# Kernel optimization log

Hardware: AMD Instinct MI355X
Metric: run time of the kernel (lower is better)

## Reference

```python
import jax, jax.numpy as jnp
import numpy as np

B, D = 8192, 128


def setup_inputs() -> dict:
    key = jax.random.key(0)
    ks = jax.random.split(key, 7)
    s = 1.0 / np.sqrt(D)  # torch Linear default init scale
    x = jax.random.normal(ks[0], (B, D), jnp.float32)
    W1 = jax.random.uniform(ks[1], (D, D), jnp.float32, -s, s)
    b1 = jax.random.uniform(ks[2], (D,), jnp.float32, -s, s)
    Wmu = jax.random.uniform(ks[3], (D, D), jnp.float32, -s, s)
    bmu = jax.random.uniform(ks[4], (D,), jnp.float32, -s, s)
    Wls = jax.random.uniform(ks[5], (D, D), jnp.float32, -s, s)
    bls = jax.random.uniform(ks[6], (D,), jnp.float32, -s, s)
    return {"x": x, "W1": W1, "b1": b1, "Wmu": Wmu, "bmu": bmu, "Wls": Wls, "bls": bls}


def reference(x, W1, b1, Wmu, bmu, Wls, bls):
    d = x.shape[1]
    mask = jnp.tril(jnp.ones((d, d), x.dtype), -1)  # strict lower triangular, as in MaskedLinear
    W1m = W1 * mask
    Wmum = Wmu * mask
    Wlsm = Wls * mask

    def step(carry, i):
        z, ldj = carry
        h = jax.nn.relu(z @ W1m.T + b1)          # [B, D] hidden (MaskedLinear + ReLU)
        # only column i of mu/logs is consumed each step -> use weight row i
        mu_i = h @ Wmum[i] + bmu[i]              # [B]
        logs_i = h @ Wlsm[i] + bls[i]            # [B]
        z = z.at[:, i].set(mu_i + x[:, i] * jnp.exp(logs_i))
        return (z, ldj + logs_i), None

    z0 = jnp.zeros_like(x)
    ldj0 = jnp.zeros(x.shape[0], x.dtype)
    (z, ldj), _ = jax.lax.scan(step, (z0, ldj0), jnp.arange(d))
    return z, ldj
```

## Files before the change

kernel.cpp:

```cpp
#include <hip/hip_runtime.h>
#include <stdint.h>

#define D 128
#define LOG2E 1.4426950408889634f
#define LN2 0.6931471805599453f

typedef float f2 __attribute__((ext_vector_type(2)));
typedef float f4 __attribute__((ext_vector_type(4)));

__device__ __forceinline__ uint16_t f2bf(float f) {
  uint32_t u = __float_as_uint(f);
  u += 0x7fffu + ((u >> 16) & 1u);
  return (uint16_t)(u >> 16);
}
__device__ __forceinline__ uint32_t pkbf(float a, float b) {
  return (uint32_t)f2bf(a) | ((uint32_t)f2bf(b) << 16);
}
__device__ __forceinline__ f2 unpkbf(uint32_t u) {
  f2 r;
  r.x = __uint_as_float(u << 16);
  r.y = __uint_as_float(u & 0xffff0000u);
  return r;
}
__device__ __forceinline__ float rdlane(float v, int l) {
  return __int_as_float(__builtin_amdgcn_readlane(__float_as_int(v), l));
}
__device__ __forceinline__ float exp2x(float v) {
#if __has_builtin(__builtin_amdgcn_exp2f)
  return __builtin_amdgcn_exp2f(v);
#else
  return exp2f(v);
#endif
}

#define WS_NEED (size_t)(3 * 2048 * 16)

__global__ __launch_bounds__(256)
void iaf_prep(const float* __restrict__ W1, const float* __restrict__ Wmu,
              const float* __restrict__ Wls, uint4* __restrict__ ws) {
  const int t = blockIdx.x * 256 + threadIdx.x;
  if (t >= 32 * 64) return;
  const int jb = t >> 6, l = t & 63;
  const int k0 = 2 * l, k1 = 2 * l + 1;
  uint32_t mm[4], ll[4], ww[4];
#pragma unroll
  for (int c = 0; c < 4; ++c) {
    const int j = jb * 4 + c;
    const float m0 = (j < k0) ? Wmu[k0 * D + j] : 0.f;
    const float m1 = (j < k1) ? Wmu[k1 * D + j] : 0.f;
    const float s0 = (j < k0) ? Wls[k0 * D + j] * LOG2E : 0.f;
    const float s1 = (j < k1) ? Wls[k1 * D + j] * LOG2E : 0.f;
    const float w0 = (j < k0) ? W1[k0 * D + j] : 0.f;
    const float w1_ = (j < k1) ? W1[k1 * D + j] : 0.f;
    mm[c] = pkbf(m0, m1);
    ll[c] = pkbf(s0, s1);
    ww[c] = pkbf(w0, w1_);
  }
  uint4 m4, l4, w4;
  m4.x = mm[0]; m4.y = mm[1]; m4.z = mm[2]; m4.w = mm[3];
  l4.x = ll[0]; l4.y = ll[1]; l4.z = ll[2]; l4.w = ll[3];
  w4.x = ww[0]; w4.y = ww[1]; w4.z = ww[2]; w4.w = ww[3];
  ws[t] = m4;
  ws[2048 + t] = l4;
  ws[4096 + t] = w4;
}

#define SEL(U, c) ((c) == 0 ? (U).x : (c) == 1 ? (U).y : (c) == 2 ? (U).z : (U).w)
#define E(V, c) (((c) & 1) ? (V).y : (V).x)

#define STEP(c)                                                         \
  {                                                                     \
    const int Ln = jb * 2 + ((c) >> 1);                                 \
    const f2 wm = unpkbf(SEL(mC, c));                                   \
    const f2 wl = unpkbf(SEL(lC, c));                                   \
    const f2 wv = unpkbf(SEL(wC, c));                                   \
    const float hA = fmaxf(E(paA, c), 0.f);                             \
    const float hB = fmaxf(E(paB, c), 0.f);                             \
    const float zA = fmaf(E(xA, c), exp2x(E(plsA, c)), E(pmuA, c));     \
    const float zB = fmaf(E(xB, c), exp2x(E(plsB, c)), E(pmuB, c));     \
    const float szA = rdlane(zA, Ln);                                   \
    const float shA = rdlane(hA, Ln);                                   \
    const float szB = rdlane(zB, Ln);                                   \
    const float shB = rdlane(hB, Ln);                                   \
    paA = __builtin_elementwise_fma((f2)szA, wv, paA);                  \
    pmuA = __builtin_elementwise_fma((f2)shA, wm, pmuA);                \
    plsA = __builtin_elementwise_fma((f2)shA, wl, plsA);                \
    paB = __builtin_elementwise_fma((f2)szB, wv, paB);                  \
    pmuB = __builtin_elementwise_fma((f2)shB, wm, pmuB);                \
    plsB = __builtin_elementwise_fma((f2)shB, wl, plsB);                \
  }

__global__ __launch_bounds__(512, 4)
void iaf_main(const float* __restrict__ x, const float* __restrict__ b1,
              const float* __restrict__ bmu, const float* __restrict__ bls,
              const uint4* __restrict__ ws, float* __restrict__ out, int B) {
  __shared__ uint4 wsh[2 * 2048];

  const int tid = threadIdx.x;
#pragma unroll
  for (int k = 0; k < 8; ++k) wsh[tid + k * 512] = ws[tid + k * 512];

  const int lane = tid & 63;
  const int wave = tid >> 6;
  const int rA = blockIdx.x * 16 + wave * 2;
  const int rB = rA + 1;
  const int l2 = lane * 2;

  const f2 xA = *(const f2*)(x + (size_t)rA * D + l2);
  const f2 xB = *(const f2*)(x + (size_t)rB * D + l2);
  f2 paA = *(const f2*)(b1 + l2);
  f2 paB = paA;
  f2 pmuA = *(const f2*)(bmu + l2);
  f2 pmuB = pmuA;
  f2 plsA = *(const f2*)(bls + l2);
  plsA.x *= LOG2E;
  plsA.y *= LOG2E;
  f2 plsB = plsA;

  const uint4* wmuP = wsh + lane;
  const uint4* wlsP = wsh + 2048 + lane;
  const uint4* w1P = ws + 4096 + lane;

  __syncthreads();

  uint4 mC = wmuP[0], lC = wlsP[0], wC = w1P[0];

#pragma unroll 1
  for (int jb = 0; jb < 32; ++jb) {
    const int adv = (jb + 1 < 32) ? 64 : 0;
    wmuP += adv;
    wlsP += adv;
    w1P += adv;
    const uint4 mN = wmuP[0];
    const uint4 lN = wlsP[0];
    const uint4 wN = w1P[0];
    STEP(0)
    STEP(1)
    STEP(2)
    STEP(3)
    mC = mN;
    lC = lN;
    wC = wN;
  }

  f2 zfA, zfB;
  zfA.x = fmaf(xA.x, exp2x(plsA.x), pmuA.x);
  zfA.y = fmaf(xA.y, exp2x(plsA.y), pmuA.y);
  zfB.x = fmaf(xB.x, exp2x(plsB.x), pmuB.x);
  zfB.y = fmaf(xB.y, exp2x(plsB.y), pmuB.y);
  *(f2*)(out + (size_t)rA * D + l2) = zfA;
  *(f2*)(out + (size_t)rB * D + l2) = zfB;

  float ldjA = plsA.x + plsA.y;
  float ldjB = plsB.x + plsB.y;
#pragma unroll
  for (int m2 = 1; m2 < 64; m2 <<= 1) {
    ldjA += __shfl_xor(ldjA, m2);
    ldjB += __shfl_xor(ldjB, m2);
  }
  if (lane == 0) {
    out[(size_t)B * D + rA] = ldjA * LN2;
    out[(size_t)B * D + rB] = ldjB * LN2;
  }
}

#define FNTHR 256
#define FRPB 16
#define W1S 136
template <int CTRL>
__device__ __forceinline__ float dppmov(float v) {
  return __int_as_float(
      __builtin_amdgcn_update_dpp(0, __float_as_int(v), CTRL, 0xf, 0xf, true));
}
#define DPP_ADD(v, ctrl) (v) += dppmov<(ctrl)>((v))
__device__ __forceinline__ f2 unpk(uint32_t u) {
  f2 r;
  r.x = __uint_as_float(u << 16);
  r.y = __uint_as_float(u & 0xffff0000u);
  return r;
}
#define RED16F(v)      \
  do {                 \
    DPP_ADD(v, 0xB1);  \
    DPP_ADD(v, 0x4E);  \
    DPP_ADD(v, 0x124); \
    DPP_ADD(v, 0x128); \
  } while (0)
#define FSTEP(I, XE, ZRE, MKE, WM0, WM1, WL0, WL1)                  \
  {                                                                 \
    const float bmu_i = bmu[(I)];                                   \
    const float bls_i = bls[(I)];                                   \
    const f2 h0 = __builtin_elementwise_max(A0, (f2)0.f);           \
    const f2 h1 = __builtin_elementwise_max(A1, (f2)0.f);           \
    const f2 h2_ = __builtin_elementwise_max(A2, (f2)0.f);          \
    const f2 h3 = __builtin_elementwise_max(A3, (f2)0.f);           \
    const f2 q0 = h0 * mk0, q1 = h1 * mk1;                          \
    const f2 q2 = h2_ * mk2, q3 = h3 * mk3;                         \
    f2 am = q0 * WM0.xy;                                            \
    f2 al = q0 * WL0.xy;                                            \
    am = __builtin_elementwise_fma(q1, WM0.zw, am);                 \
    al = __builtin_elementwise_fma(q1, WL0.zw, al);                 \
    am = __builtin_elementwise_fma(q2, WM1.xy, am);                 \
    al = __builtin_elementwise_fma(q2, WL1.xy, al);                 \
    am = __builtin_elementwise_fma(q3, WM1.zw, am);                 \
    al = __builtin_elementwise_fma(q3, WL1.zw, al);                 \
    float mu_p = am.x + am.y;                                       \
    float ls_p = al.x + al.y;                                       \
    {                                                               \
      const int pfr = ((I) + 2 < D) ? (I) + 2 : D - 1;              \
      WM0 = *(const f4*)(wmup + pfr * D);                           \
      WM1 = *(const f4*)(wmup + pfr * D + 4);                       \
      WL0 = *(const f4*)(wlsp + pfr * D);                           \
      WL1 = *(const f4*)(wlsp + pfr * D + 4);                       \
    }                                                               \
    RED16F(mu_p);                                                   \
    RED16F(ls_p);                                                   \
    const float mu_t = mu_p + bmu_i;                                \
    const float ls_t = ls_p + bls_i;                                \
    const float zi = fmaf((XE), __expf(ls_t), mu_t);                \
    ldj += ls_t;                                                    \
    const uint4 wv = *(const uint4*)(w1p + (I)*W1S);                \
    if (own) {                                                      \
      ZRE = zi;                                                     \
      MKE = 1.f;                                                    \
    }                                                               \
    f2 zz;                                                          \
    zz.x = zi;                                                      \
    zz.y = zi;                                                      \
    A0 = __builtin_elementwise_fma(zz, unpk(wv.x), A0);             \
    A1 = __builtin_elementwise_fma(zz, unpk(wv.y), A1);             \
    A2 = __builtin_elementwise_fma(zz, unpk(wv.z), A2);             \
    A3 = __builtin_elementwise_fma(zz, unpk(wv.w), A3);             \
  }

__global__ __launch_bounds__(FNTHR, 2)
void iaf_fb(const float* __restrict__ x, const float* __restrict__ W1,
            const float* __restrict__ b1, const float* __restrict__ Wmu,
            const float* __restrict__ bmu, const float* __restrict__ Wls,
            const float* __restrict__ bls, float* __restrict__ out, int B) {
  __shared__ uint16_t w1c[D * W1S];
  const int tid = threadIdx.x;
  for (int idx = tid; idx < D * D; idx += FNTHR) {
    const int p = idx >> 7, q = idx & (D - 1);
    w1c[q * W1S + p] = f2bf((p > q) ? W1[idx] : 0.f);
  }
  __syncthreads();
  const int lane = tid & 63;
  const int m = lane & 15;
  const int row = blockIdx.x * FRPB + (tid >> 4);
  const float* __restrict__ xp = x + (size_t)row * D;
  const float* __restrict__ wmup = Wmu + m * 8;
  const float* __restrict__ wlsp = Wls + m * 8;
  const uint16_t* __restrict__ w1p = w1c + m * 8;
  f2 A0, A1, A2, A3;
  {
    const f4 t0 = *(const f4*)(b1 + m * 8);
    const f4 t1 = *(const f4*)(b1 + m * 8 + 4);
    A0 = t0.xy; A1 = t0.zw; A2 = t1.xy; A3 = t1.zw;
  }
  f2 mk0 = (f2)0.f, mk1 = (f2)0.f, mk2 = (f2)0.f, mk3 = (f2)0.f;
  float zr0 = 0, zr1 = 0, zr2 = 0, zr3 = 0, zr4 = 0, zr5 = 0, zr6 = 0, zr7 = 0;
  float ldj = 0.f;
  f4 wmA0 = *(const f4*)(wmup);
  f4 wmA1 = *(const f4*)(wmup + 4);
  f4 wlA0 = *(const f4*)(wlsp);
  f4 wlA1 = *(const f4*)(wlsp + 4);
  f4 wmB0 = *(const f4*)(wmup + D);
  f4 wmB1 = *(const f4*)(wmup + D + 4);
  f4 wlB0 = *(const f4*)(wlsp + D);
  f4 wlB1 = *(const f4*)(wlsp + D + 4);
  f4 x4a = *(const f4*)(xp);
  f4 x4b;
  for (int ib = 0; ib < 16; ++ib) {
    const int i0 = ib * 8;
    const bool own = (m == ib);
    x4b = *(const f4*)(xp + i0 + 4);
    FSTEP(i0 + 0, x4a.x, zr0, mk0.x, wmA0, wmA1, wlA0, wlA1);
    FSTEP(i0 + 1, x4a.y, zr1, mk0.y, wmB0, wmB1, wlB0, wlB1);
    FSTEP(i0 + 2, x4a.z, zr2, mk1.x, wmA0, wmA1, wlA0, wlA1);
    FSTEP(i0 + 3, x4a.w, zr3, mk1.y, wmB0, wmB1, wlB0, wlB1);
    {
      const int nx = (i0 + 8 < D) ? i0 + 8 : D - 4;
      x4a = *(const f4*)(xp + nx);
    }
    FSTEP(i0 + 4, x4b.x, zr4, mk2.x, wmA0, wmA1, wlA0, wlA1);
    FSTEP(i0 + 5, x4b.y, zr5, mk2.y, wmB0, wmB1, wlB0, wlB1);
    FSTEP(i0 + 6, x4b.z, zr6, mk3.x, wmA0, wmA1, wlA0, wlA1);
    FSTEP(i0 + 7, x4b.w, zr7, mk3.y, wmB0, wmB1, wlB0, wlB1);
  }
  f4 o0, o1;
  o0.x = zr0; o0.y = zr1; o0.z = zr2; o0.w = zr3;
  o1.x = zr4; o1.y = zr5; o1.z = zr6; o1.w = zr7;
  float* zo = out + (size_t)row * D + m * 8;
  *(f4*)(zo) = o0;
  *(f4*)(zo + 4) = o1;
  if (m == 0) out[(size_t)B * D + row] = ldj;
}

extern "C" void kernel_launch(void* const* d_in, const int* in_sizes, int n_in,
                              void* d_out, int out_size, void* d_ws, size_t ws_size,
                              hipStream_t stream) {
  const float* x   = (const float*)d_in[0];
  const float* W1  = (const float*)d_in[1];
  const float* b1  = (const float*)d_in[2];
  const float* Wmu = (const float*)d_in[3];
  const float* bmu = (const float*)d_in[4];
  const float* Wls = (const float*)d_in[5];
  const float* bls = (const float*)d_in[6];
  float* out = (float*)d_out;

  const int B = in_sizes[0] / D;

  if (ws_size >= WS_NEED) {
    iaf_prep<<<8, 256, 0, stream>>>(W1, Wmu, Wls, (uint4*)d_ws);
    const int grid = (B + 15) / 16;
    iaf_main<<<grid, 512, 0, stream>>>(x, b1, bmu, bls, (const uint4*)d_ws, out, B);
  } else {
    const int grid = (B + FRPB - 1) / FRPB;
    iaf_fb<<<grid, FNTHR, 0, stream>>>(x, W1, b1, Wmu, bmu, Wls, bls, out, B);
  }
}
```

Before: 39.22 us.

## Process four rows per wave and double-buffer weight loads per iteration

```diff
diff --git a/kernel.cpp b/kernel.cpp
--- a/kernel.cpp
+++ b/kernel.cpp
@@ -68,29 +68,43 @@
 #define SEL(U, c) ((c) == 0 ? (U).x : (c) == 1 ? (U).y : (c) == 2 ? (U).z : (U).w)
 #define E(V, c) (((c) & 1) ? (V).y : (V).x)
 
-#define STEP(c)                                                         \
-  {                                                                     \
-    const int Ln = jb * 2 + ((c) >> 1);                                 \
-    const f2 wm = unpkbf(SEL(mC, c));                                   \
-    const f2 wl = unpkbf(SEL(lC, c));                                   \
-    const f2 wv = unpkbf(SEL(wC, c));                                   \
-    const float hA = fmaxf(E(paA, c), 0.f);                             \
-    const float hB = fmaxf(E(paB, c), 0.f);                             \
-    const float zA = fmaf(E(xA, c), exp2x(E(plsA, c)), E(pmuA, c));     \
-    const float zB = fmaf(E(xB, c), exp2x(E(plsB, c)), E(pmuB, c));     \
-    const float szA = rdlane(zA, Ln);                                   \
-    const float shA = rdlane(hA, Ln);                                   \
-    const float szB = rdlane(zB, Ln);                                   \
-    const float shB = rdlane(hB, Ln);                                   \
-    paA = __builtin_elementwise_fma((f2)szA, wv, paA);                  \
-    pmuA = __builtin_elementwise_fma((f2)shA, wm, pmuA);                \
-    plsA = __builtin_elementwise_fma((f2)shA, wl, plsA);                \
-    paB = __builtin_elementwise_fma((f2)szB, wv, paB);                  \
-    pmuB = __builtin_elementwise_fma((f2)shB, wm, pmuB);                \
-    plsB = __builtin_elementwise_fma((f2)shB, wl, plsB);                \
-  }
-
-__global__ __launch_bounds__(512, 4)
+#define STEP(c, M4, L4, W4, JB)                                       \
+  {                                                                   \
+    const int Ln = (JB) * 2 + ((c) >> 1);                             \
+    const f2 wm = unpkbf(SEL(M4, c));                                 \
+    const f2 wl = unpkbf(SEL(L4, c));                                 \
+    const f2 wv = unpkbf(SEL(W4, c));                                 \
+    const float hA = fmaxf(E(paA, c), 0.f);                           \
+    const float hB = fmaxf(E(paB, c), 0.f);                           \
+    const float hC = fmaxf(E(paC, c), 0.f);                           \
+    const float hD = fmaxf(E(paD, c), 0.f);                           \
+    const float zA = fmaf(E(xA, c), exp2x(E(plsA, c)), E(pmuA, c));   \
+    const float zB = fmaf(E(xB, c), exp2x(E(plsB, c)), E(pmuB, c));   \
+    const float zC = fmaf(E(xC, c), exp2x(E(plsC, c)), E(pmuC, c));   \
+    const float zD = fmaf(E(xD, c), exp2x(E(plsD, c)), E(pmuD, c));   \
+    const float szA = rdlane(zA, Ln);                                 \
+    const float shA = rdlane(hA, Ln);                                 \
+    const float szB = rdlane(zB, Ln);                                 \
+    const float shB = rdlane(hB, Ln);                                 \
+    const float szC = rdlane(zC, Ln);                                 \
+    const float shC = rdlane(hC, Ln);                                 \
+    const float szD = rdlane(zD, Ln);                                 \
+    const float shD = rdlane(hD, Ln);                                 \
+    paA = __builtin_elementwise_fma((f2)szA, wv, paA);                \
+    pmuA = __builtin_elementwise_fma((f2)shA, wm, pmuA);              \
+    plsA = __builtin_elementwise_fma((f2)shA, wl, plsA);              \
+    paB = __builtin_elementwise_fma((f2)szB, wv, paB);                \
+    pmuB = __builtin_elementwise_fma((f2)shB, wm, pmuB);              \
+    plsB = __builtin_elementwise_fma((f2)shB, wl, plsB);              \
+    paC = __builtin_elementwise_fma((f2)szC, wv, paC);                \
+    pmuC = __builtin_elementwise_fma((f2)shC, wm, pmuC);              \
+    plsC = __builtin_elementwise_fma((f2)shC, wl, plsC);              \
+    paD = __builtin_elementwise_fma((f2)szD, wv, paD);                \
+    pmuD = __builtin_elementwise_fma((f2)shD, wm, pmuD);              \
+    plsD = __builtin_elementwise_fma((f2)shD, wl, plsD);              \
+  }
+
+__global__ __launch_bounds__(256, 2)
 void iaf_main(const float* __restrict__ x, const float* __restrict__ b1,
               const float* __restrict__ bmu, const float* __restrict__ bls,
               const uint4* __restrict__ ws, float* __restrict__ out, int B) {
@@ -98,24 +112,25 @@
 
   const int tid = threadIdx.x;
 #pragma unroll
-  for (int k = 0; k < 8; ++k) wsh[tid + k * 512] = ws[tid + k * 512];
+  for (int k = 0; k < 16; ++k) wsh[tid + k * 256] = ws[tid + k * 256];
 
   const int lane = tid & 63;
   const int wave = tid >> 6;
-  const int rA = blockIdx.x * 16 + wave * 2;
-  const int rB = rA + 1;
+  const int rA = blockIdx.x * 16 + wave * 4;
   const int l2 = lane * 2;
 
   const f2 xA = *(const f2*)(x + (size_t)rA * D + l2);
-  const f2 xB = *(const f2*)(x + (size_t)rB * D + l2);
+  const f2 xB = *(const f2*)(x + (size_t)(rA + 1) * D + l2);
+  const f2 xC = *(const f2*)(x + (size_t)(rA + 2) * D + l2);
+  const f2 xD = *(const f2*)(x + (size_t)(rA + 3) * D + l2);
   f2 paA = *(const f2*)(b1 + l2);
-  f2 paB = paA;
+  f2 paB = paA, paC = paA, paD = paA;
   f2 pmuA = *(const f2*)(bmu + l2);
-  f2 pmuB = pmuA;
+  f2 pmuB = pmuA, pmuC = pmuA, pmuD = pmuA;
   f2 plsA = *(const f2*)(bls + l2);
   plsA.x *= LOG2E;
   plsA.y *= LOG2E;
-  f2 plsB = plsA;
+  f2 plsB = plsA, plsC = plsA, plsD = plsA;
 
   const uint4* wmuP = wsh + lane;
   const uint4* wlsP = wsh + 2048 + lane;
@@ -123,44 +138,60 @@
 
   __syncthreads();
 
-  uint4 mC = wmuP[0], lC = wlsP[0], wC = w1P[0];
+  uint4 m0 = wmuP[0], l0 = wlsP[0], w0 = w1P[0];
 
 #pragma unroll 1
-  for (int jb = 0; jb < 32; ++jb) {
-    const int adv = (jb + 1 < 32) ? 64 : 0;
+  for (int jb = 0; jb < 32; jb += 2) {
+    const uint4 m1 = wmuP[64];
+    const uint4 l1 = wlsP[64];
+    const uint4 w1v = w1P[64];
+    STEP(0, m0, l0, w0, jb)
+    STEP(1, m0, l0, w0, jb)
+    STEP(2, m0, l0, w0, jb)
+    STEP(3, m0, l0, w0, jb)
+    const int adv = (jb + 2 < 32) ? 128 : 0;
     wmuP += adv;
     wlsP += adv;
     w1P += adv;
-    const uint4 mN = wmuP[0];
-    const uint4 lN = wlsP[0];
-    const uint4 wN = w1P[0];
-    STEP(0)
-    STEP(1)
-    STEP(2)
-    STEP(3)
-    mC = mN;
-    lC = lN;
-    wC = wN;
-  }
-
-  f2 zfA, zfB;
-  zfA.x = fmaf(xA.x, exp2x(plsA.x), pmuA.x);
-  zfA.y = fmaf(xA.y, exp2x(plsA.y), pmuA.y);
-  zfB.x = fmaf(xB.x, exp2x(plsB.x), pmuB.x);
-  zfB.y = fmaf(xB.y, exp2x(plsB.y), pmuB.y);
-  *(f2*)(out + (size_t)rA * D + l2) = zfA;
-  *(f2*)(out + (size_t)rB * D + l2) = zfB;
+    m0 = wmuP[0];
+    l0 = wlsP[0];
+    w0 = w1P[0];
+    STEP(0, m1, l1, w1v, jb + 1)
+    STEP(1, m1, l1, w1v, jb + 1)
+    STEP(2, m1, l1, w1v, jb + 1)
+    STEP(3, m1, l1, w1v, jb + 1)
+  }
+
+  f2 zf;
+  zf.x = fmaf(xA.x, exp2x(plsA.x), pmuA.x);
+  zf.y = fmaf(xA.y, exp2x(plsA.y), pmuA.y);
+  *(f2*)(out + (size_t)rA * D + l2) = zf;
+  zf.x = fmaf(xB.x, exp2x(plsB.x), pmuB.x);
+  zf.y = fmaf(xB.y, exp2x(plsB.y), pmuB.y);
+  *(f2*)(out + (size_t)(rA + 1) * D + l2) = zf;
+  zf.x = fmaf(xC.x, exp2x(plsC.x), pmuC.x);
+  zf.y = fmaf(xC.y, exp2x(plsC.y), pmuC.y);
+  *(f2*)(out + (size_t)(rA + 2) * D + l2) = zf;
+  zf.x = fmaf(xD.x, exp2x(plsD.x), pmuD.x);
+  zf.y = fmaf(xD.y, exp2x(plsD.y), pmuD.y);
+  *(f2*)(out + (size_t)(rA + 3) * D + l2) = zf;
 
   float ldjA = plsA.x + plsA.y;
   float ldjB = plsB.x + plsB.y;
+  float ldjC = plsC.x + plsC.y;
+  float ldjD = plsD.x + plsD.y;
 #pragma unroll
   for (int m2 = 1; m2 < 64; m2 <<= 1) {
     ldjA += __shfl_xor(ldjA, m2);
     ldjB += __shfl_xor(ldjB, m2);
+    ldjC += __shfl_xor(ldjC, m2);
+    ldjD += __shfl_xor(ldjD, m2);
   }
   if (lane == 0) {
     out[(size_t)B * D + rA] = ldjA * LN2;
-    out[(size_t)B * D + rB] = ldjB * LN2;
+    out[(size_t)B * D + rA + 1] = ldjB * LN2;
+    out[(size_t)B * D + rA + 2] = ldjC * LN2;
+    out[(size_t)B * D + rA + 3] = ldjD * LN2;
   }
 }
 
@@ -314,7 +345,7 @@
   if (ws_size >= WS_NEED) {
     iaf_prep<<<8, 256, 0, stream>>>(W1, Wmu, Wls, (uint4*)d_ws);
     const int grid = (B + 15) / 16;
-    iaf_main<<<grid, 512, 0, stream>>>(x, b1, bmu, bls, (const uint4*)d_ws, out, B);
+    iaf_main<<<grid, 256, 0, stream>>>(x, b1, bmu, bls, (const uint4*)d_ws, out, B);
   } else {
     const int grid = (B + FRPB - 1) / FRPB;
     iaf_fb<<<grid, FNTHR, 0, stream>>>(x, W1, b1, Wmu, bmu, Wls, bls, out, B);
```

Measured after the change: 36.55 us. -6.8%, faster.
